# Performance work log

Measured on AMD Instinct MI355X. Metric: run time of the kernel, lower is better.

The kernel has to match this reference:

```python
import jax, jax.numpy as jnp
import numpy as np

K = 16
N = 32
NUM_WORDS = 2 ** K  # 65536


def build_codebook(G):
    """Faithful translation of MinDistanceDecoder.init_codebook.

    Returns (possible_words [2^k, k], possible_codewords [2^k, n],
             possible_codewords_llrs [2^k, n]) in float32.
    """
    Gf = G.astype(jnp.float32)
    # coefs = round(2 ** linspace(1, k, k)) = [2, 4, ..., 2^k]
    coefs = jnp.round(2.0 ** jnp.linspace(1.0, float(K), K))  # [k]
    # linspace(0, 2^k-1, 2^k) hits exact integers; floor is identity here
    idx = jnp.floor(jnp.linspace(0.0, float(NUM_WORDS) - 1.0, NUM_WORDS))  # [2^k]
    pw = idx[:, None] % coefs[None, :]  # [2^k, k]
    sub = jnp.concatenate([jnp.zeros((NUM_WORDS, 1), jnp.float32), pw[:, :-1]], axis=-1)
    possible_words = (pw - sub) / (coefs / 2.0)  # binary bits, LSB-first
    possible_codewords = (possible_words @ Gf) % 2.0  # [2^k, n]
    possible_codewords_llrs = -1.0 * (possible_codewords * 2.0 - 1.0)  # +/-1 BPSK LLR signs
    return possible_words, possible_codewords, possible_codewords_llrs


def setup_inputs() -> dict:
    key = jax.random.key(0)
    k1, k2 = jax.random.split(key)
    noisy_symbols = jax.random.normal(k1, (64, N), dtype=jnp.float32)
    G = jax.random.randint(k2, (K, N), 0, 2, dtype=jnp.int32)
    sigma2 = jnp.ones((1,), dtype=jnp.float32)
    return {"noisy_symbols": noisy_symbols, "G": G, "sigma2": sigma2}


def reference(noisy_symbols, G, sigma2):
    possible_words, possible_codewords, cw_llrs = build_codebook(G)
    llrs = -4.0 * noisy_symbols.astype(jnp.float32) / sigma2  # [B, n]
    max_abs = jnp.max(jnp.abs(llrs))  # global max over broadcast tensor == max over llrs
    # mean |llr - max_abs * codeword_llr| per (batch, codeword): [B, 2^k]
    dist = jnp.mean(jnp.abs(llrs[:, None, :] - max_abs * cw_llrs[None, :, :]), axis=-1)
    best = jnp.argmin(dist, axis=-1)  # [B]
    # return_words=True -> gather message words
    return possible_words[best]  # [B, k]
```

## Files before the change

kernel.cpp:

```cpp
#include <hip/hip_runtime.h>
#include <stdint.h>

#define B 64
#define N 32
#define K 16
#define NUM_WORDS 65536
#define NBLK 256
#define WPB 256
#define NTHR 512
#define LLR_PAD 65

typedef unsigned long long u64;

static __device__ __forceinline__ u64 umax64(u64 a, u64 b) { return a > b ? a : b; }

__global__ __launch_bounds__(NTHR) void mdd_corr(
    const float* __restrict__ noisy,
    const int* __restrict__ G,
    const float* __restrict__ sigma2,
    u64* __restrict__ ws)
{
    __shared__ uint32_t g_rows[K];
    __shared__ __align__(16) uint32_t cw_lds[WPB];
    __shared__ float T_lds[4 * 128 * 64];
    __shared__ float llr_t[N * LLR_PAD];
    __shared__ float bestf_lds[8 * 64];
    __shared__ uint32_t bestw_lds[8 * 64];

    const int tid = threadIdx.x;
    const int l = tid & 63;
    const int wv = tid >> 6;

    if (tid < K) {
        const int4* G4 = reinterpret_cast<const int4*>(G) + tid * 8;
        uint32_t r = 0;
        #pragma unroll
        for (int m = 0; m < 8; ++m) {
            int4 gv = G4[m];
            r |= (uint32_t)(gv.x & 1) << (4 * m + 0);
            r |= (uint32_t)(gv.y & 1) << (4 * m + 1);
            r |= (uint32_t)(gv.z & 1) << (4 * m + 2);
            r |= (uint32_t)(gv.w & 1) << (4 * m + 3);
        }
        g_rows[tid] = r;
    }

    const float scale = -4.0f / sigma2[0];
    for (int i = tid; i < B * N; i += NTHR) {
        int n = i & 31, bb = i >> 5;
        llr_t[n * LLR_PAD + bb] = scale * noisy[i];
    }
    __syncthreads();

    if (tid < WPB) {
        uint32_t w = blockIdx.x * WPB + tid;
        uint32_t cw = 0;
        #pragma unroll
        for (int k = 0; k < K; ++k)
            cw ^= g_rows[k] & (0u - ((w >> k) & 1u));
        cw_lds[tid] = cw;
    }

    {
        const int g = wv & 3, h = wv >> 2;
        float l0 = llr_t[(7 * g + 0) * LLR_PAD + l];
        float l1 = llr_t[(7 * g + 1) * LLR_PAD + l];
        float l2 = llr_t[(7 * g + 2) * LLR_PAD + l];
        float l3 = llr_t[(7 * g + 3) * LLR_PAD + l];
        float l4 = llr_t[(7 * g + 4) * LLR_PAD + l];
        float l5 = llr_t[(7 * g + 5) * LLR_PAD + l];
        float l6 = llr_t[(7 * g + 6) * LLR_PAD + l];
        float l6s = h ? -l6 : l6;
        float P[4] = { l0 + l1, -l0 + l1, l0 - l1, -l0 - l1 };
        float A[8];
        #pragma unroll
        for (int a = 0; a < 8; ++a)
            A[a] = (a & 4) ? (P[a & 3] - l2) : (P[a & 3] + l2);
        float Q[4] = { l3 + l4, -l3 + l4, l3 - l4, -l3 - l4 };
        float R[8];
        #pragma unroll
        for (int r = 0; r < 8; ++r)
            R[r] = (r & 4) ? (Q[r & 3] - l5) : (Q[r & 3] + l5);
        float Cp[8];
        #pragma unroll
        for (int c = 0; c < 8; ++c)
            Cp[c] = R[c] + l6s;
        float* Tg = &T_lds[g * 8192 + h * 64 * 64 + l];
        #pragma unroll
        for (int j = 0; j < 64; ++j)
            Tg[j * 64] = A[j & 7] + Cp[j >> 3];
    }

    uint32_t lau0 = __float_as_uint(llr_t[28 * LLR_PAD + l]);
    uint32_t lau1 = __float_as_uint(llr_t[29 * LLR_PAD + l]);
    uint32_t lau2 = __float_as_uint(llr_t[30 * LLR_PAD + l]);
    uint32_t lau3 = __float_as_uint(llr_t[31 * LLR_PAD + l]);
    __syncthreads();

    const uint4* cw4 = reinterpret_cast<const uint4*>(cw_lds);
    const float* Tl = &T_lds[l];
    float bestf = -INFINITY;
    uint32_t bestw = 0;
    const uint32_t wbase = blockIdx.x * WPB + wv * 32;

    #pragma unroll
    for (int wq = 0; wq < 8; ++wq) {
        uint4 c4 = cw4[wv * 8 + wq];
        #pragma unroll
        for (int e = 0; e < 4; ++e) {
            uint32_t cw = (e == 0) ? c4.x : (e == 1) ? c4.y : (e == 2) ? c4.z : c4.w;
            float r0 = Tl[0 * 8192 + ((cw >> 0) & 127u) * 64];
            float r1 = Tl[1 * 8192 + ((cw >> 7) & 127u) * 64];
            float r2 = Tl[2 * 8192 + ((cw >> 14) & 127u) * 64];
            float r3 = Tl[3 * 8192 + ((cw >> 21) & 127u) * 64];
            float v0 = __uint_as_float(lau0 ^ ((cw << 3) & 0x80000000u));
            float v1 = __uint_as_float(lau1 ^ ((cw << 2) & 0x80000000u));
            float v2 = __uint_as_float(lau2 ^ ((cw << 1) & 0x80000000u));
            float v3 = __uint_as_float(lau3 ^ ((cw << 0) & 0x80000000u));
            float c = ((r0 + r1) + (r2 + r3)) + ((v0 + v1) + (v2 + v3));
            uint32_t w = wbase + wq * 4 + e;
            bool g = c > bestf;
            bestw = g ? w : bestw;
            bestf = g ? c : bestf;
        }
    }

    bestf_lds[wv * 64 + l] = bestf;
    bestw_lds[wv * 64 + l] = bestw;
    __syncthreads();

    if (tid < B) {
        float f = bestf_lds[tid];
        uint32_t w = bestw_lds[tid];
        #pragma unroll
        for (int v = 1; v < 8; ++v) {
            float f2 = bestf_lds[v * 64 + tid];
            uint32_t w2 = bestw_lds[v * 64 + tid];
            bool g = f2 > f;
            w = g ? w2 : w;
            f = g ? f2 : f;
        }
        uint32_t bits = __float_as_uint(f);
        uint32_t mono = (bits & 0x80000000u) ? ~bits : (bits | 0x80000000u);
        u64 key = ((u64)mono << 16) | (u64)(0xFFFFu - w);
        ws[(size_t)tid * NBLK + blockIdx.x] = key;
    }
}

__global__ __launch_bounds__(64) void mdd_out(
    const u64* __restrict__ ws,
    float* __restrict__ out)
{
    const int b = blockIdx.x;
    const int t = threadIdx.x;
    const u64* p = ws + (size_t)b * NBLK;

    u64 m = umax64(umax64(p[t], p[t + 64]), umax64(p[t + 128], p[t + 192]));
    #pragma unroll
    for (int off = 32; off > 0; off >>= 1) {
        u64 o = __shfl_xor(m, off, 64);
        m = umax64(m, o);
    }
    uint32_t w = 0xFFFFu - (uint32_t)(m & 0xFFFFull);
    if (t < K) out[b * K + t] = (float)((w >> t) & 1u);
}

extern "C" void kernel_launch(void* const* d_in, const int* in_sizes, int n_in,
                              void* d_out, int out_size, void* d_ws, size_t ws_size,
                              hipStream_t stream) {
    const float* noisy = (const float*)d_in[0];
    const int* G = (const int*)d_in[1];
    const float* sigma2 = (const float*)d_in[2];
    float* out = (float*)d_out;
    u64* ws = (u64*)d_ws;

    (void)in_sizes; (void)n_in; (void)out_size; (void)ws_size;

    mdd_corr<<<NBLK, NTHR, 0, stream>>>(noisy, G, sigma2, ws);
    mdd_out<<<B, 64, 0, stream>>>(ws, out);
}
```

Measured before the change: 13.45 us.

## Shrink lookup tables to 6-bit chunks and drop LDS staging of LLRs

Result: slower. 15.21 us (+13.1%).

```diff
diff --git a/kernel.cpp b/kernel.cpp
--- a/kernel.cpp
+++ b/kernel.cpp
@@ -8,7 +8,6 @@
 #define NBLK 256
 #define WPB 256
 #define NTHR 512
-#define LLR_PAD 65
 
 typedef unsigned long long u64;
 
@@ -20,81 +19,59 @@
     const float* __restrict__ sigma2,
     u64* __restrict__ ws)
 {
-    __shared__ uint32_t g_rows[K];
     __shared__ __align__(16) uint32_t cw_lds[WPB];
-    __shared__ float T_lds[4 * 128 * 64];
-    __shared__ float llr_t[N * LLR_PAD];
+    __shared__ float T_lds[4 * 64 * 64];
     __shared__ float bestf_lds[8 * 64];
     __shared__ uint32_t bestw_lds[8 * 64];
 
     const int tid = threadIdx.x;
     const int l = tid & 63;
     const int wv = tid >> 6;
-
-    if (tid < K) {
-        const int4* G4 = reinterpret_cast<const int4*>(G) + tid * 8;
-        uint32_t r = 0;
-        #pragma unroll
-        for (int m = 0; m < 8; ++m) {
-            int4 gv = G4[m];
-            r |= (uint32_t)(gv.x & 1) << (4 * m + 0);
-            r |= (uint32_t)(gv.y & 1) << (4 * m + 1);
-            r |= (uint32_t)(gv.z & 1) << (4 * m + 2);
-            r |= (uint32_t)(gv.w & 1) << (4 * m + 3);
-        }
-        g_rows[tid] = r;
-    }
+    const int g = wv & 3;
+    const int h = wv >> 2;
 
     const float scale = -4.0f / sigma2[0];
-    for (int i = tid; i < B * N; i += NTHR) {
-        int n = i & 31, bb = i >> 5;
-        llr_t[n * LLR_PAD + bb] = scale * noisy[i];
-    }
-    __syncthreads();
 
-    if (tid < WPB) {
+    if (wv < 4) {
+        uint32_t grows[K];
+        #pragma unroll
+        for (int k = 0; k < K; k += 2) {
+            int gv = G[k * N + l];
+            u64 m = __ballot(gv & 1);
+            grows[k] = (uint32_t)m;
+            grows[k + 1] = (uint32_t)(m >> 32);
+        }
         uint32_t w = blockIdx.x * WPB + tid;
         uint32_t cw = 0;
         #pragma unroll
         for (int k = 0; k < K; ++k)
-            cw ^= g_rows[k] & (0u - ((w >> k) & 1u));
+            cw ^= grows[k] & (0u - ((w >> k) & 1u));
         cw_lds[tid] = cw;
     }
 
     {
-        const int g = wv & 3, h = wv >> 2;
-        float l0 = llr_t[(7 * g + 0) * LLR_PAD + l];
-        float l1 = llr_t[(7 * g + 1) * LLR_PAD + l];
-        float l2 = llr_t[(7 * g + 2) * LLR_PAD + l];
-        float l3 = llr_t[(7 * g + 3) * LLR_PAD + l];
-        float l4 = llr_t[(7 * g + 4) * LLR_PAD + l];
-        float l5 = llr_t[(7 * g + 5) * LLR_PAD + l];
-        float l6 = llr_t[(7 * g + 6) * LLR_PAD + l];
-        float l6s = h ? -l6 : l6;
-        float P[4] = { l0 + l1, -l0 + l1, l0 - l1, -l0 - l1 };
-        float A[8];
+        const float* nb = noisy + l * N + 6 * g;
+        float l0 = scale * nb[0];
+        float l1 = scale * nb[1];
+        float l2 = scale * nb[2];
+        float l3 = scale * nb[3];
+        float l4 = scale * nb[4];
+        float l5 = scale * nb[5];
+        float l5s = h ? -l5 : l5;
+        float P01[4] = { l0 + l1, -l0 + l1, l0 - l1, -l0 - l1 };
+        float P23[4] = { l2 + l3, -l2 + l3, l2 - l3, -l2 - l3 };
+        float Q0 = l4 + l5s, Q1 = -l4 + l5s;
+        float* Tp = &T_lds[g * 4096 + h * 32 * 64 + l];
         #pragma unroll
-        for (int a = 0; a < 8; ++a)
-            A[a] = (a & 4) ? (P[a & 3] - l2) : (P[a & 3] + l2);
-        float Q[4] = { l3 + l4, -l3 + l4, l3 - l4, -l3 - l4 };
-        float R[8];
-        #pragma unroll
-        for (int r = 0; r < 8; ++r)
-            R[r] = (r & 4) ? (Q[r & 3] - l5) : (Q[r & 3] + l5);
-        float Cp[8];
-        #pragma unroll
-        for (int c = 0; c < 8; ++c)
-            Cp[c] = R[c] + l6s;
-        float* Tg = &T_lds[g * 8192 + h * 64 * 64 + l];
-        #pragma unroll
-        for (int j = 0; j < 64; ++j)
-            Tg[j * 64] = A[j & 7] + Cp[j >> 3];
+        for (int j = 0; j < 32; ++j)
+            Tp[j * 64] = (P01[j & 3] + P23[(j >> 2) & 3]) + ((j & 16) ? Q1 : Q0);
     }
 
-    uint32_t lau0 = __float_as_uint(llr_t[28 * LLR_PAD + l]);
-    uint32_t lau1 = __float_as_uint(llr_t[29 * LLR_PAD + l]);
-    uint32_t lau2 = __float_as_uint(llr_t[30 * LLR_PAD + l]);
-    uint32_t lau3 = __float_as_uint(llr_t[31 * LLR_PAD + l]);
+    uint32_t lau[8];
+    #pragma unroll
+    for (int v = 0; v < 8; ++v)
+        lau[v] = __float_as_uint(scale * noisy[l * N + 24 + v]);
+
     __syncthreads();
 
     const uint4* cw4 = reinterpret_cast<const uint4*>(cw_lds);
@@ -109,19 +86,24 @@
         #pragma unroll
         for (int e = 0; e < 4; ++e) {
             uint32_t cw = (e == 0) ? c4.x : (e == 1) ? c4.y : (e == 2) ? c4.z : c4.w;
-            float r0 = Tl[0 * 8192 + ((cw >> 0) & 127u) * 64];
-            float r1 = Tl[1 * 8192 + ((cw >> 7) & 127u) * 64];
-            float r2 = Tl[2 * 8192 + ((cw >> 14) & 127u) * 64];
-            float r3 = Tl[3 * 8192 + ((cw >> 21) & 127u) * 64];
-            float v0 = __uint_as_float(lau0 ^ ((cw << 3) & 0x80000000u));
-            float v1 = __uint_as_float(lau1 ^ ((cw << 2) & 0x80000000u));
-            float v2 = __uint_as_float(lau2 ^ ((cw << 1) & 0x80000000u));
-            float v3 = __uint_as_float(lau3 ^ ((cw << 0) & 0x80000000u));
-            float c = ((r0 + r1) + (r2 + r3)) + ((v0 + v1) + (v2 + v3));
+            float r0 = Tl[0 * 4096 + ((cw >> 0) & 63u) * 64];
+            float r1 = Tl[1 * 4096 + ((cw >> 6) & 63u) * 64];
+            float r2 = Tl[2 * 4096 + ((cw >> 12) & 63u) * 64];
+            float r3 = Tl[3 * 4096 + ((cw >> 18) & 63u) * 64];
+            float v0 = __uint_as_float(lau[0] ^ ((cw << 7) & 0x80000000u));
+            float v1 = __uint_as_float(lau[1] ^ ((cw << 6) & 0x80000000u));
+            float v2 = __uint_as_float(lau[2] ^ ((cw << 5) & 0x80000000u));
+            float v3 = __uint_as_float(lau[3] ^ ((cw << 4) & 0x80000000u));
+            float v4 = __uint_as_float(lau[4] ^ ((cw << 3) & 0x80000000u));
+            float v5 = __uint_as_float(lau[5] ^ ((cw << 2) & 0x80000000u));
+            float v6 = __uint_as_float(lau[6] ^ ((cw << 1) & 0x80000000u));
+            float v7 = __uint_as_float(lau[7] ^ ((cw << 0) & 0x80000000u));
+            float c = ((r0 + r1) + (r2 + r3))
+                    + (((v0 + v1) + (v2 + v3)) + ((v4 + v5) + (v6 + v7)));
             uint32_t w = wbase + wq * 4 + e;
-            bool g = c > bestf;
-            bestw = g ? w : bestw;
-            bestf = g ? c : bestf;
+            bool gt = c > bestf;
+            bestw = gt ? w : bestw;
+            bestf = gt ? c : bestf;
         }
     }
 
@@ -136,9 +118,9 @@
         for (int v = 1; v < 8; ++v) {
             float f2 = bestf_lds[v * 64 + tid];
             uint32_t w2 = bestw_lds[v * 64 + tid];
-            bool g = f2 > f;
-            w = g ? w2 : w;
-            f = g ? f2 : f;
+            bool gt = f2 > f;
+            w = gt ? w2 : w;
+            f = gt ? f2 : f;
         }
         uint32_t bits = __float_as_uint(f);
         uint32_t mono = (bits & 0x80000000u) ? ~bits : (bits | 0x80000000u);
```
